# Kernel tuning notes

Hardware: AMD Instinct MI355X
Metric: run time of the kernel (lower is better)

## Reference

```python
import jax, jax.numpy as jnp
import numpy as np

B, T, FIN, D = 8, 512, 256, 128


def setup_inputs() -> dict:
    key = jax.random.key(0)
    ks = jax.random.split(key, 12)
    s = lambda fan_in: 1.0 / np.sqrt(fan_in)
    return {
        "x": jax.random.normal(ks[0], (B, T, FIN), jnp.float32),
        "S0": jnp.zeros((B, 1, D, D), jnp.float32),
        "Z0": jnp.zeros((B, 1, D), jnp.float32),
        "gamma": jnp.ones((FIN,), jnp.float32),
        "beta": jnp.zeros((FIN,), jnp.float32),
        "Wk": jax.random.normal(ks[1], (FIN, D), jnp.float32) * s(FIN),
        "Wq": jax.random.normal(ks[2], (FIN, D), jnp.float32) * s(FIN),
        "Wv": jax.random.normal(ks[3], (FIN, D), jnp.float32) * s(FIN),
        "W1": jax.random.normal(ks[4], (D, D), jnp.float32) * s(D),
        "b1": jnp.zeros((D,), jnp.float32),
        "W2": jax.random.normal(ks[5], (D, D), jnp.float32) * s(D),
        "b2": jnp.zeros((D,), jnp.float32),
        "Ws": jax.random.normal(ks[6], (FIN, D), jnp.float32) * s(FIN),
        "bs": jnp.zeros((D,), jnp.float32),
    }


def reference(x, S0, Z0, gamma, beta, Wk, Wq, Wv, W1, b1, W2, b2, Ws, bs):
    CLAMP = 1e20
    # LayerNorm over feature dim
    mu = jnp.mean(x, axis=-1, keepdims=True)
    var = jnp.var(x, axis=-1, keepdims=True)
    xn = (x - mu) / jnp.sqrt(var + 1e-5) * gamma + beta
    # phi(x) = elu(x) + 1
    K = jax.nn.elu(xn @ Wk) + 1.0  # [B,T,D]
    Q = jax.nn.elu(xn @ Wq) + 1.0  # [B,T,D]
    V = xn @ Wv                     # [B,T,D]
    # outer-product state recurrence via cumsum (faithful to original)
    outer = jnp.einsum('bti,btj->btij', K, V)            # [B,T,D,D]
    S = jnp.clip(jnp.cumsum(outer, axis=1), -CLAMP, CLAMP) + S0  # [B,T,D,D]
    Z = jnp.clip(jnp.cumsum(K, axis=1), -CLAMP, CLAMP) + Z0      # [B,T,D]
    numerator = jnp.einsum('bti,btil->btl', Q, S)        # [B,T,D]
    denominator = jnp.einsum('bti,bti->bt', Q, Z)[..., None] + 1e-5
    out = numerator / denominator
    # FFN: relu(relu(out W1 + b1) W2 + b2)
    out = jax.nn.relu(jax.nn.relu(out @ W1 + b1) @ W2 + b2)
    # residual shortcut from normed input
    out = out + xn @ Ws + bs
    S_out = S.reshape(B, T, D * D)
    return out, S_out, Z
```

## Files before the change

kernel.cpp:

```cpp
#include <hip/hip_runtime.h>


constexpr int BB = 8, TT = 512, FIN_ = 256, DD = 128;
constexpr int NROW = BB * TT;
constexpr int CLEN = 64, NCH = 8;
constexpr float CLAMPV = 1e20f;

typedef float f4v __attribute__((ext_vector_type(4)));

__global__ __launch_bounds__(256) void gemm_qkvs(
    const float* __restrict__ x,
    const float* __restrict__ gamma, const float* __restrict__ beta,
    const float* __restrict__ Wk, const float* __restrict__ Wq,
    const float* __restrict__ Wv, const float* __restrict__ Ws,
    const float* __restrict__ bs,
    float* __restrict__ Kb, float* __restrict__ Qb,
    float* __restrict__ Vb, float* __restrict__ Rb)
{
  int ct = blockIdx.x, rt = blockIdx.y;
  int mat = ct >> 1, cb = (ct & 1) * 64;
  const float* W = (mat == 0) ? Wk : (mat == 1) ? Wq : (mat == 2) ? Wv : Ws;
  float* Ob      = (mat == 0) ? Kb : (mat == 1) ? Qb : (mat == 2) ? Vb : Rb;
  __shared__ float As[2][16][64];
  __shared__ float Bs[2][16][64];
  __shared__ float mu_s[64], rs_s[64];
  int tid = threadIdx.x;
  {
    int row = tid >> 2, q = tid & 3;
    const float* xr = &x[(rt * 64 + row) * FIN_ + q * 64];
    float sum = 0.f, sq = 0.f;
#pragma unroll
    for (int u = 0; u < 16; u++) {
      float4 v = *(const float4*)&xr[u * 4];
      sum += v.x + v.y + v.z + v.w;
      sq  += v.x * v.x + v.y * v.y + v.z * v.z + v.w * v.w;
    }
    sum += __shfl_xor(sum, 1); sq += __shfl_xor(sq, 1);
    sum += __shfl_xor(sum, 2); sq += __shfl_xor(sq, 2);
    if (q == 0) {
      float mu = sum * (1.0f / FIN_);
      float var = sq * (1.0f / FIN_) - mu * mu;
      mu_s[row] = mu;
      rs_s[row] = rsqrtf(var + 1e-5f);
    }
  }
  __syncthreads();
  int tn = tid & 15, tm = tid >> 4;
  int lm = tid >> 2, lq = tid & 3;
  int lk = tid >> 4, ln4 = (tid & 15) * 4;
  float acc[4][4] = {};
  float mu = mu_s[lm], rs = rs_s[lm];
  float4 xa = *(const float4*)&x[(rt * 64 + lm) * FIN_ + lq * 4];
  float4 ga = *(const float4*)&gamma[lq * 4];
  float4 be = *(const float4*)&beta[lq * 4];
  float4 wb = *(const float4*)&W[lk * DD + cb + ln4];
  int cur = 0;
  for (int k0 = 0; k0 < FIN_; k0 += 16) {
    As[cur][lq * 4 + 0][lm] = (xa.x - mu) * rs * ga.x + be.x;
    As[cur][lq * 4 + 1][lm] = (xa.y - mu) * rs * ga.y + be.y;
    As[cur][lq * 4 + 2][lm] = (xa.z - mu) * rs * ga.z + be.z;
    As[cur][lq * 4 + 3][lm] = (xa.w - mu) * rs * ga.w + be.w;
    *(float4*)&Bs[cur][lk][ln4] = wb;
    if (k0 + 16 < FIN_) {
      xa = *(const float4*)&x[(rt * 64 + lm) * FIN_ + k0 + 16 + lq * 4];
      ga = *(const float4*)&gamma[k0 + 16 + lq * 4];
      be = *(const float4*)&beta[k0 + 16 + lq * 4];
      wb = *(const float4*)&W[(k0 + 16 + lk) * DD + cb + ln4];
    }
    __syncthreads();
#pragma unroll
    for (int k = 0; k < 16; k++) {
      float4 a = *(const float4*)&As[cur][k][tm * 4];
      float4 b = *(const float4*)&Bs[cur][k][tn * 4];
      float ar[4] = {a.x, a.y, a.z, a.w};
      float br[4] = {b.x, b.y, b.z, b.w};
#pragma unroll
      for (int i = 0; i < 4; i++)
#pragma unroll
        for (int j = 0; j < 4; j++) acc[i][j] += ar[i] * br[j];
    }
    cur ^= 1;
  }
#pragma unroll
  for (int i = 0; i < 4; i++) {
    int row = rt * 64 + tm * 4 + i;
    int col = cb + tn * 4;
    float vals[4];
#pragma unroll
    for (int j = 0; j < 4; j++) {
      float v = acc[i][j];
      if (mat <= 1) v = (v > 0.f) ? v + 1.f : expf(v);
      else if (mat == 3) v += bs[col + j];
      vals[j] = v;
    }
    *(float4*)&Ob[row * DD + col] = make_float4(vals[0], vals[1], vals[2], vals[3]);
  }
}

__global__ __launch_bounds__(256) void prefix_kernel(
    const float* __restrict__ Kb, const float* __restrict__ Vb,
    const float* __restrict__ S0, const float* __restrict__ Z0,
    float* __restrict__ prefS, float* __restrict__ prefz)
{
  int jt = blockIdx.x, it = blockIdx.y, b = blockIdx.z;
  int i0 = it * 16, j0 = jt * 32;
  __shared__ float Ks[2][CLEN][16];
  __shared__ float Vs[2][CLEN][32];
  int tid = threadIdx.x;
  int il = tid >> 4, jl = tid & 15;
  float2 s0v = *(const float2*)&S0[b * DD * DD + (i0 + il) * DD + j0 + jl * 2];
  float acc0 = 0.f, acc1 = 0.f;
  float zacc = 0.f;
  float z0v = (jt == 0 && tid < 16) ? Z0[b * DD + i0 + tid] : 0.f;
  {
    const float* Kc = Kb + (b * TT) * DD;
    const float* Vc = Vb + (b * TT) * DD;
    int t = tid >> 2, i4 = (tid & 3) * 4;
    *(float4*)&Ks[0][t][i4] = *(const float4*)&Kc[t * DD + i0 + i4];
#pragma unroll
    for (int u = 0; u < 2; u++) {
      int idx = u * 256 + tid;
      int tv = idx >> 3, j4 = (idx & 7) * 4;
      *(float4*)&Vs[0][tv][j4] = *(const float4*)&Vc[tv * DD + j0 + j4];
    }
  }
  int cur = 0;
  for (int c = 0; c < NCH; c++) {
    __syncthreads();
    float4 kq, vq0, vq1;
    if (c + 1 < NCH) {
      const float* Kc = Kb + (b * TT + (c + 1) * CLEN) * DD;
      const float* Vc = Vb + (b * TT + (c + 1) * CLEN) * DD;
      kq  = *(const float4*)&Kc[(tid >> 2) * DD + i0 + (tid & 3) * 4];
      vq0 = *(const float4*)&Vc[(tid >> 3) * DD + j0 + (tid & 7) * 4];
      int idx = 256 + tid;
      vq1 = *(const float4*)&Vc[(idx >> 3) * DD + j0 + (idx & 7) * 4];
    }
    float2 op = make_float2(acc0 + s0v.x, acc1 + s0v.y);
    *(float2*)&prefS[(size_t)(b * NCH + c) * DD * DD + (i0 + il) * DD + j0 + jl * 2] = op;
    if (jt == 0 && tid < 16)
      prefz[(b * NCH + c) * DD + i0 + tid] = zacc + z0v;
#pragma unroll 8
    for (int t = 0; t < CLEN; t++) {
      float k = Ks[cur][t][il];
      float2 v2 = *(const float2*)&Vs[cur][t][jl * 2];
      acc0 += k * v2.x;
      acc1 += k * v2.y;
    }
    if (jt == 0 && tid < 16) {
      float z = 0.f;
#pragma unroll 8
      for (int t = 0; t < CLEN; t++) z += Ks[cur][t][tid];
      zacc += z;
    }
    if (c + 1 < NCH) {
      *(float4*)&Ks[cur ^ 1][tid >> 2][(tid & 3) * 4] = kq;
      *(float4*)&Vs[cur ^ 1][tid >> 3][(tid & 7) * 4] = vq0;
      int idx = 256 + tid;
      *(float4*)&Vs[cur ^ 1][idx >> 3][(idx & 7) * 4] = vq1;
    }
    cur ^= 1;
  }
}

union MegaSmem {
  struct {
    float KsT[DD][CLEN + 2];
    float Qs[8][132];
    float sc[8][CLEN + 2];
    float zeff[DD];
    float den[8];
    float As[8][132];
    float H1[8][132];
  } a;
  struct {
    float Vs[CLEN][DD];
    float Ksm[CLEN][16];
  } s;
};

__global__ __launch_bounds__(256) void mega_kernel(
    const float* __restrict__ Kb, const float* __restrict__ Qb,
    const float* __restrict__ Vb, const float* __restrict__ prefS,
    const float* __restrict__ prefz, const float* __restrict__ Rb,
    const float* __restrict__ W1, const float* __restrict__ b1,
    const float* __restrict__ W2, const float* __restrict__ b2,
    float* __restrict__ Zout, float* __restrict__ out_main,
    float* __restrict__ Sout)
{
  __shared__ MegaSmem sm;
  int c = blockIdx.y, b = blockIdx.z, tid = threadIdx.x;
  const float* Kc = Kb + (b * TT + c * CLEN) * DD;
  const float* Vc = Vb + (b * TT + c * CLEN) * DD;

  if (blockIdx.x >= 8) {
    int i0 = (blockIdx.x - 8) * 16;
#pragma unroll
    for (int u = 0; u < 8; u++) {
      int idx = u * 256 + tid;
      int t = idx >> 5, c4 = (idx & 31) * 4;
      *(float4*)&sm.s.Vs[t][c4] = *(const float4*)&Vc[t * DD + c4];
    }
#pragma unroll
    for (int u = 0; u < 4; u++) {
      int idx = u * 256 + tid;
      int t = idx >> 4, r = idx & 15;
      sm.s.Ksm[t][r] = Kc[t * DD + i0 + r];
    }
    __syncthreads();
    int irow = tid >> 5, jq = tid & 31;
    int j = jq * 4;
    size_t pbase = (size_t)(b * NCH + c) * DD * DD;
    float4 prefA = *(const float4*)&prefS[pbase + (i0 + irow) * DD + j];
    float4 prefB = *(const float4*)&prefS[pbase + (i0 + 8 + irow) * DD + j];
    float4 accA = make_float4(0.f, 0.f, 0.f, 0.f);
    float4 accB = make_float4(0.f, 0.f, 0.f, 0.f);
    float* SoA = Sout + (size_t)(b * TT + c * CLEN) * (DD * DD) + (i0 + irow) * DD + j;
    float* SoB = SoA + 8 * DD;
#pragma unroll 2
    for (int t = 0; t < CLEN; t++) {
      float4 v4 = *(const float4*)&sm.s.Vs[t][j];
      float kA = sm.s.Ksm[t][irow];
      float kB = sm.s.Ksm[t][irow + 8];
      accA.x += kA * v4.x; accA.y += kA * v4.y;
      accA.z += kA * v4.z; accA.w += kA * v4.w;
      f4v oA;
      oA.x = fminf(fmaxf(prefA.x + accA.x, -CLAMPV), CLAMPV);
      oA.y = fminf(fmaxf(prefA.y + accA.y, -CLAMPV), CLAMPV);
      oA.z = fminf(fmaxf(prefA.z + accA.z, -CLAMPV), CLAMPV);
      oA.w = fminf(fmaxf(prefA.w + accA.w, -CLAMPV), CLAMPV);
      __builtin_nontemporal_store(oA, (f4v*)&SoA[(size_t)t * (DD * DD)]);
      accB.x += kB * v4.x; accB.y += kB * v4.y;
      accB.z += kB * v4.z; accB.w += kB * v4.w;
      f4v oB;
      oB.x = fminf(fmaxf(prefB.x + accB.x, -CLAMPV), CLAMPV);
      oB.y = fminf(fmaxf(prefB.y + accB.y, -CLAMPV), CLAMPV);
      oB.z = fminf(fmaxf(prefB.z + accB.z, -CLAMPV), CLAMPV);
      oB.w = fminf(fmaxf(prefB.w + accB.w, -CLAMPV), CLAMPV);
      __builtin_nontemporal_store(oB, (f4v*)&SoB[(size_t)t * (DD * DD)]);
    }
    return;
  }

  int sub = blockIdx.x;
  int t0 = sub * 8;
  int tlim = t0 + 8;
  const float* Qc = Qb + (b * TT + c * CLEN) * DD;
  for (int idx = tid; idx < tlim * 32; idx += 256) {
    int t = idx >> 5, c4 = (idx & 31) * 4;
    float4 vv = *(const float4*)&Kc[t * DD + c4];
    sm.a.KsT[c4 + 0][t] = vv.x; sm.a.KsT[c4 + 1][t] = vv.y;
    sm.a.KsT[c4 + 2][t] = vv.z; sm.a.KsT[c4 + 3][t] = vv.w;
  }
  {
    int r = tid >> 5, c4 = (tid & 31) * 4;
    *(float4*)&sm.a.Qs[r][c4] = *(const float4*)&Qc[(t0 + r) * DD + c4];
  }
  if (tid < DD) sm.a.zeff[tid] = prefz[(b * NCH + c) * DD + tid];
  __syncthreads();
  {
    int tm = tid >> 5, tn = tid & 31;
    int tau0 = tn * 2;
    if (tau0 < tlim) {
      float s0 = 0.f, s1 = 0.f;
#pragma unroll 8
      for (int k = 0; k < DD; k++) {
        float q = sm.a.Qs[tm][k];
        float2 kk = *(const float2*)&sm.a.KsT[k][tau0];
        s0 += q * kk.x;
        s1 += q * kk.y;
      }
      int t = t0 + tm;
      sm.a.sc[tm][tau0]     = (tau0     <= t) ? s0 : 0.f;
      sm.a.sc[tm][tau0 + 1] = (tau0 + 1 <= t) ? s1 : 0.f;
    }
  }
  __syncthreads();
  {
    int r = tid >> 5, g = tid & 31;
    int t = t0 + r;
    float p = 0.f;
    for (int tau = g; tau <= t; tau += 32) p += sm.a.sc[r][tau];
#pragma unroll 4
    for (int k = g; k < DD; k += 32) p += sm.a.Qs[r][k] * sm.a.zeff[k];
#pragma unroll
    for (int off = 1; off < 32; off <<= 1) p += __shfl_xor(p, off);
    if (g == 0) sm.a.den[r] = p + 1e-5f;
  }
  __syncthreads();
  int tl = tid & 31, r = tid >> 5;
  int l0 = tl * 4;
  {
    float n0[4] = {};
#pragma unroll 4
    for (int tau = 0; tau < tlim; tau++) {
      float4 v4 = *(const float4*)&Vc[tau * DD + l0];
      float s = sm.a.sc[r][tau];
      n0[0] += s * v4.x; n0[1] += s * v4.y; n0[2] += s * v4.z; n0[3] += s * v4.w;
    }
    const float* P = prefS + (size_t)(b * NCH + c) * DD * DD;
#pragma unroll 4
    for (int i = 0; i < DD; i++) {
      float4 p4 = *(const float4*)&P[i * DD + l0];
      float q = sm.a.Qs[r][i];
      n0[0] += q * p4.x; n0[1] += q * p4.y; n0[2] += q * p4.z; n0[3] += q * p4.w;
    }
    float dd = sm.a.den[r];
    *(float4*)&sm.a.As[r][l0] =
        make_float4(n0[0] / dd, n0[1] / dd, n0[2] / dd, n0[3] / dd);
  }
  if (sub == 7 && tid < DD) {
    int i = tid;
    float a = sm.a.zeff[i];
    for (int t = 0; t < CLEN; t++) {
      a += sm.a.KsT[i][t];
      a = fminf(fmaxf(a, -CLAMPV), CLAMPV);
      __builtin_nontemporal_store(a, &Zout[(size_t)(b * TT + c * CLEN + t) * DD + i]);
    }
  }
  __syncthreads();
  {
    float a1[4] = {};
#pragma unroll 8
    for (int k = 0; k < DD; k++) {
      float4 w = *(const float4*)&W1[k * DD + l0];
      float a = sm.a.As[r][k];
      a1[0] += a * w.x; a1[1] += a * w.y; a1[2] += a * w.z; a1[3] += a * w.w;
    }
    float4 bv = *(const float4*)&b1[l0];
    float4 h;
    h.x = fmaxf(a1[0] + bv.x, 0.f);
    h.y = fmaxf(a1[1] + bv.y, 0.f);
    h.z = fmaxf(a1[2] + bv.z, 0.f);
    h.w = fmaxf(a1[3] + bv.w, 0.f);
    *(float4*)&sm.a.H1[r][l0] = h;
  }
  __syncthreads();
  {
    float a2[4] = {};
#pragma unroll 8
    for (int k = 0; k < DD; k++) {
      float4 w = *(const float4*)&W2[k * DD + l0];
      float a = sm.a.H1[r][k];
      a2[0] += a * w.x; a2[1] += a * w.y; a2[2] += a * w.z; a2[3] += a * w.w;
    }
    int grow = b * TT + c * CLEN + t0 + r;
    float4 b2v = *(const float4*)&b2[l0];
    float4 rv = *(const float4*)&Rb[grow * DD + l0];
    float4 o;
    o.x = fmaxf(a2[0] + b2v.x, 0.f) + rv.x;
    o.y = fmaxf(a2[1] + b2v.y, 0.f) + rv.y;
    o.z = fmaxf(a2[2] + b2v.z, 0.f) + rv.z;
    o.w = fmaxf(a2[3] + b2v.w, 0.f) + rv.w;
    *(float4*)&out_main[grow * DD + l0] = o;
  }
}

extern "C" void kernel_launch(void* const* d_in, const int* in_sizes, int n_in,
                              void* d_out, int out_size, void* d_ws, size_t ws_size,
                              hipStream_t stream)
{
  const float* x     = (const float*)d_in[0];
  const float* S0    = (const float*)d_in[1];
  const float* Z0    = (const float*)d_in[2];
  const float* gamma = (const float*)d_in[3];
  const float* beta  = (const float*)d_in[4];
  const float* Wk    = (const float*)d_in[5];
  const float* Wq    = (const float*)d_in[6];
  const float* Wv    = (const float*)d_in[7];
  const float* W1    = (const float*)d_in[8];
  const float* b1    = (const float*)d_in[9];
  const float* W2    = (const float*)d_in[10];
  const float* b2    = (const float*)d_in[11];
  const float* Ws    = (const float*)d_in[12];
  const float* bs    = (const float*)d_in[13];

  float* out_main = (float*)d_out;
  float* Sout = out_main + NROW * DD;
  float* Zout = Sout + (size_t)NROW * DD * DD;

  float* ws_f   = (float*)d_ws;
  float* Kb     = ws_f;
  float* Qb     = Kb + 524288;
  float* Vb     = Qb + 524288;
  float* Rb     = Vb + 524288;
  float* prefS  = Rb + 524288;
  float* prefz  = prefS + 1048576;

  gemm_qkvs<<<dim3(8, 64), 256, 0, stream>>>(x, gamma, beta, Wk, Wq, Wv, Ws, bs,
                                             Kb, Qb, Vb, Rb);
  prefix_kernel<<<dim3(4, 8, BB), 256, 0, stream>>>(Kb, Vb, S0, Z0, prefS, prefz);
  mega_kernel<<<dim3(16, NCH, BB), 256, 0, stream>>>(Kb, Qb, Vb, prefS, prefz, Rb,
                                                     W1, b1, W2, b2,
                                                     Zout, out_main, Sout);
}
```

Baseline: 373.9 us.

## Fuse S-state output writes into prefix scan kernel, drop S blocks from mega kernel

Moves the per-timestep cumulative state writes into the chunk-sequential prefix kernel, which now also emits the clamped running sum for every timestep. The mega kernel loses its state-writing blocks and becomes an attention/FFN-only kernel. The prefix grid is retiled to 8x64 tiles with 256 blocks. The aim is to avoid reloading the chunk prefix, at the cost of serialising the large output write across chunks within each block and using narrower float2 stores.

```diff
diff --git a/kernel.cpp b/kernel.cpp
--- a/kernel.cpp
+++ b/kernel.cpp
@@ -7,6 +7,7 @@
 constexpr float CLAMPV = 1e20f;
 
 typedef float f4v __attribute__((ext_vector_type(4)));
+typedef float f2v __attribute__((ext_vector_type(2)));
 
 __global__ __launch_bounds__(256) void gemm_qkvs(
     const float* __restrict__ x,
@@ -100,148 +101,99 @@
 __global__ __launch_bounds__(256) void prefix_kernel(
     const float* __restrict__ Kb, const float* __restrict__ Vb,
     const float* __restrict__ S0, const float* __restrict__ Z0,
-    float* __restrict__ prefS, float* __restrict__ prefz)
+    float* __restrict__ prefS, float* __restrict__ prefz,
+    float* __restrict__ Sout)
 {
-  int jt = blockIdx.x, it = blockIdx.y, b = blockIdx.z;
-  int i0 = it * 16, j0 = jt * 32;
-  __shared__ float Ks[2][CLEN][16];
-  __shared__ float Vs[2][CLEN][32];
+  int jh = blockIdx.x, it = blockIdx.y, b = blockIdx.z;
+  int i0 = it * 8, j0 = jh * 64;
+  __shared__ float Ks[2][CLEN][8];
+  __shared__ float Vs[2][CLEN][64];
   int tid = threadIdx.x;
-  int il = tid >> 4, jl = tid & 15;
+  int il = tid >> 5, jl = tid & 31;
   float2 s0v = *(const float2*)&S0[b * DD * DD + (i0 + il) * DD + j0 + jl * 2];
-  float acc0 = 0.f, acc1 = 0.f;
-  float zacc = 0.f;
-  float z0v = (jt == 0 && tid < 16) ? Z0[b * DD + i0 + tid] : 0.f;
+  float acc0 = 0.f, acc1 = 0.f, zacc = 0.f;
+  float z0v = (jh == 0 && tid < 8) ? Z0[b * DD + i0 + tid] : 0.f;
   {
     const float* Kc = Kb + (b * TT) * DD;
     const float* Vc = Vb + (b * TT) * DD;
-    int t = tid >> 2, i4 = (tid & 3) * 4;
-    *(float4*)&Ks[0][t][i4] = *(const float4*)&Kc[t * DD + i0 + i4];
-#pragma unroll
-    for (int u = 0; u < 2; u++) {
+    int t = tid >> 2, i2 = (tid & 3) * 2;
+    *(float2*)&Ks[0][t][i2] = *(const float2*)&Kc[t * DD + i0 + i2];
+#pragma unroll
+    for (int u = 0; u < 4; u++) {
       int idx = u * 256 + tid;
-      int tv = idx >> 3, j4 = (idx & 7) * 4;
+      int tv = idx >> 4, j4 = (idx & 15) * 4;
       *(float4*)&Vs[0][tv][j4] = *(const float4*)&Vc[tv * DD + j0 + j4];
     }
   }
   int cur = 0;
   for (int c = 0; c < NCH; c++) {
     __syncthreads();
-    float4 kq, vq0, vq1;
+    float2 kq;
+    float4 vq[4];
     if (c + 1 < NCH) {
       const float* Kc = Kb + (b * TT + (c + 1) * CLEN) * DD;
       const float* Vc = Vb + (b * TT + (c + 1) * CLEN) * DD;
-      kq  = *(const float4*)&Kc[(tid >> 2) * DD + i0 + (tid & 3) * 4];
-      vq0 = *(const float4*)&Vc[(tid >> 3) * DD + j0 + (tid & 7) * 4];
-      int idx = 256 + tid;
-      vq1 = *(const float4*)&Vc[(idx >> 3) * DD + j0 + (idx & 7) * 4];
-    }
-    float2 op = make_float2(acc0 + s0v.x, acc1 + s0v.y);
-    *(float2*)&prefS[(size_t)(b * NCH + c) * DD * DD + (i0 + il) * DD + j0 + jl * 2] = op;
-    if (jt == 0 && tid < 16)
+      kq = *(const float2*)&Kc[(tid >> 2) * DD + i0 + (tid & 3) * 2];
+#pragma unroll
+      for (int u = 0; u < 4; u++) {
+        int idx = u * 256 + tid;
+        vq[u] = *(const float4*)&Vc[(idx >> 4) * DD + j0 + (idx & 15) * 4];
+      }
+    }
+    float p0 = acc0 + s0v.x, p1 = acc1 + s0v.y;
+    *(float2*)&prefS[(size_t)(b * NCH + c) * DD * DD + (i0 + il) * DD + j0 + jl * 2] =
+        make_float2(p0, p1);
+    if (jh == 0 && tid < 8)
       prefz[(b * NCH + c) * DD + i0 + tid] = zacc + z0v;
-#pragma unroll 8
+    float w0 = 0.f, w1 = 0.f;
+    float* So = Sout + (size_t)(b * TT + c * CLEN) * (DD * DD) + (i0 + il) * DD + j0 + jl * 2;
+#pragma unroll 4
     for (int t = 0; t < CLEN; t++) {
       float k = Ks[cur][t][il];
       float2 v2 = *(const float2*)&Vs[cur][t][jl * 2];
-      acc0 += k * v2.x;
-      acc1 += k * v2.y;
-    }
-    if (jt == 0 && tid < 16) {
+      acc0 += k * v2.x; acc1 += k * v2.y;
+      w0 += k * v2.x;   w1 += k * v2.y;
+      f2v o2;
+      o2.x = fminf(fmaxf(p0 + w0, -CLAMPV), CLAMPV);
+      o2.y = fminf(fmaxf(p1 + w1, -CLAMPV), CLAMPV);
+      __builtin_nontemporal_store(o2, (f2v*)&So[(size_t)t * (DD * DD)]);
+    }
+    if (jh == 0 && tid < 8) {
       float z = 0.f;
 #pragma unroll 8
       for (int t = 0; t < CLEN; t++) z += Ks[cur][t][tid];
       zacc += z;
     }
     if (c + 1 < NCH) {
-      *(float4*)&Ks[cur ^ 1][tid >> 2][(tid & 3) * 4] = kq;
-      *(float4*)&Vs[cur ^ 1][tid >> 3][(tid & 7) * 4] = vq0;
-      int idx = 256 + tid;
-      *(float4*)&Vs[cur ^ 1][idx >> 3][(idx & 7) * 4] = vq1;
+      *(float2*)&Ks[cur ^ 1][tid >> 2][(tid & 3) * 2] = kq;
+#pragma unroll
+      for (int u = 0; u < 4; u++) {
+        int idx = u * 256 + tid;
+        *(float4*)&Vs[cur ^ 1][idx >> 4][(idx & 15) * 4] = vq[u];
+      }
     }
     cur ^= 1;
   }
 }
 
-union MegaSmem {
-  struct {
-    float KsT[DD][CLEN + 2];
-    float Qs[8][132];
-    float sc[8][CLEN + 2];
-    float zeff[DD];
-    float den[8];
-    float As[8][132];
-    float H1[8][132];
-  } a;
-  struct {
-    float Vs[CLEN][DD];
-    float Ksm[CLEN][16];
-  } s;
-};
-
-__global__ __launch_bounds__(256) void mega_kernel(
+__global__ __launch_bounds__(256) void attn_kernel(
     const float* __restrict__ Kb, const float* __restrict__ Qb,
     const float* __restrict__ Vb, const float* __restrict__ prefS,
     const float* __restrict__ prefz, const float* __restrict__ Rb,
     const float* __restrict__ W1, const float* __restrict__ b1,
     const float* __restrict__ W2, const float* __restrict__ b2,
-    float* __restrict__ Zout, float* __restrict__ out_main,
-    float* __restrict__ Sout)
+    float* __restrict__ Zout, float* __restrict__ out_main)
 {
-  __shared__ MegaSmem sm;
+  __shared__ float KsT[DD][CLEN + 2];
+  __shared__ float Qs[8][132];
+  __shared__ float sc[8][CLEN + 2];
+  __shared__ float zeff[DD];
+  __shared__ float den[8];
+  __shared__ float Ao[8][132];
+  __shared__ float H1[8][132];
   int c = blockIdx.y, b = blockIdx.z, tid = threadIdx.x;
   const float* Kc = Kb + (b * TT + c * CLEN) * DD;
   const float* Vc = Vb + (b * TT + c * CLEN) * DD;
-
-  if (blockIdx.x >= 8) {
-    int i0 = (blockIdx.x - 8) * 16;
-#pragma unroll
-    for (int u = 0; u < 8; u++) {
-      int idx = u * 256 + tid;
-      int t = idx >> 5, c4 = (idx & 31) * 4;
-      *(float4*)&sm.s.Vs[t][c4] = *(const float4*)&Vc[t * DD + c4];
-    }
-#pragma unroll
-    for (int u = 0; u < 4; u++) {
-      int idx = u * 256 + tid;
-      int t = idx >> 4, r = idx & 15;
-      sm.s.Ksm[t][r] = Kc[t * DD + i0 + r];
-    }
-    __syncthreads();
-    int irow = tid >> 5, jq = tid & 31;
-    int j = jq * 4;
-    size_t pbase = (size_t)(b * NCH + c) * DD * DD;
-    float4 prefA = *(const float4*)&prefS[pbase + (i0 + irow) * DD + j];
-    float4 prefB = *(const float4*)&prefS[pbase + (i0 + 8 + irow) * DD + j];
-    float4 accA = make_float4(0.f, 0.f, 0.f, 0.f);
-    float4 accB = make_float4(0.f, 0.f, 0.f, 0.f);
-    float* SoA = Sout + (size_t)(b * TT + c * CLEN) * (DD * DD) + (i0 + irow) * DD + j;
-    float* SoB = SoA + 8 * DD;
-#pragma unroll 2
-    for (int t = 0; t < CLEN; t++) {
-      float4 v4 = *(const float4*)&sm.s.Vs[t][j];
-      float kA = sm.s.Ksm[t][irow];
-      float kB = sm.s.Ksm[t][irow + 8];
-      accA.x += kA * v4.x; accA.y += kA * v4.y;
-      accA.z += kA * v4.z; accA.w += kA * v4.w;
-      f4v oA;
-      oA.x = fminf(fmaxf(prefA.x + accA.x, -CLAMPV), CLAMPV);
-      oA.y = fminf(fmaxf(prefA.y + accA.y, -CLAMPV), CLAMPV);
-      oA.z = fminf(fmaxf(prefA.z + accA.z, -CLAMPV), CLAMPV);
-      oA.w = fminf(fmaxf(prefA.w + accA.w, -CLAMPV), CLAMPV);
-      __builtin_nontemporal_store(oA, (f4v*)&SoA[(size_t)t * (DD * DD)]);
-      accB.x += kB * v4.x; accB.y += kB * v4.y;
-      accB.z += kB * v4.z; accB.w += kB * v4.w;
-      f4v oB;
-      oB.x = fminf(fmaxf(prefB.x + accB.x, -CLAMPV), CLAMPV);
-      oB.y = fminf(fmaxf(prefB.y + accB.y, -CLAMPV), CLAMPV);
-      oB.z = fminf(fmaxf(prefB.z + accB.z, -CLAMPV), CLAMPV);
-      oB.w = fminf(fmaxf(prefB.w + accB.w, -CLAMPV), CLAMPV);
-      __builtin_nontemporal_store(oB, (f4v*)&SoB[(size_t)t * (DD * DD)]);
-    }
-    return;
-  }
-
   int sub = blockIdx.x;
   int t0 = sub * 8;
   int tlim = t0 + 8;
@@ -249,14 +201,14 @@
   for (int idx = tid; idx < tlim * 32; idx += 256) {
     int t = idx >> 5, c4 = (idx & 31) * 4;
     float4 vv = *(const float4*)&Kc[t * DD + c4];
-    sm.a.KsT[c4 + 0][t] = vv.x; sm.a.KsT[c4 + 1][t] = vv.y;
-    sm.a.KsT[c4 + 2][t] = vv.z; sm.a.KsT[c4 + 3][t] = vv.w;
+    KsT[c4 + 0][t] = vv.x; KsT[c4 + 1][t] = vv.y;
+    KsT[c4 + 2][t] = vv.z; KsT[c4 + 3][t] = vv.w;
   }
   {
     int r = tid >> 5, c4 = (tid & 31) * 4;
-    *(float4*)&sm.a.Qs[r][c4] = *(const float4*)&Qc[(t0 + r) * DD + c4];
-  }
-  if (tid < DD) sm.a.zeff[tid] = prefz[(b * NCH + c) * DD + tid];
+    *(float4*)&Qs[r][c4] = *(const float4*)&Qc[(t0 + r) * DD + c4];
+  }
+  if (tid < DD) zeff[tid] = prefz[(b * NCH + c) * DD + tid];
   __syncthreads();
   {
     int tm = tid >> 5, tn = tid & 31;
@@ -265,14 +217,14 @@
       float s0 = 0.f, s1 = 0.f;
 #pragma unroll 8
       for (int k = 0; k < DD; k++) {
-        float q = sm.a.Qs[tm][k];
-        float2 kk = *(const float2*)&sm.a.KsT[k][tau0];
+        float q = Qs[tm][k];
+        float2 kk = *(const float2*)&KsT[k][tau0];
         s0 += q * kk.x;
         s1 += q * kk.y;
       }
       int t = t0 + tm;
-      sm.a.sc[tm][tau0]     = (tau0     <= t) ? s0 : 0.f;
-      sm.a.sc[tm][tau0 + 1] = (tau0 + 1 <= t) ? s1 : 0.f;
+      sc[tm][tau0]     = (tau0     <= t) ? s0 : 0.f;
+      sc[tm][tau0 + 1] = (tau0 + 1 <= t) ? s1 : 0.f;
     }
   }
   __syncthreads();
@@ -280,12 +232,12 @@
     int r = tid >> 5, g = tid & 31;
     int t = t0 + r;
     float p = 0.f;
-    for (int tau = g; tau <= t; tau += 32) p += sm.a.sc[r][tau];
+    for (int tau = g; tau <= t; tau += 32) p += sc[r][tau];
 #pragma unroll 4
-    for (int k = g; k < DD; k += 32) p += sm.a.Qs[r][k] * sm.a.zeff[k];
+    for (int k = g; k < DD; k += 32) p += Qs[r][k] * zeff[k];
 #pragma unroll
     for (int off = 1; off < 32; off <<= 1) p += __shfl_xor(p, off);
-    if (g == 0) sm.a.den[r] = p + 1e-5f;
+    if (g == 0) den[r] = p + 1e-5f;
   }
   __syncthreads();
   int tl = tid & 31, r = tid >> 5;
@@ -295,25 +247,24 @@
 #pragma unroll 4
     for (int tau = 0; tau < tlim; tau++) {
       float4 v4 = *(const float4*)&Vc[tau * DD + l0];
-      float s = sm.a.sc[r][tau];
+      float s = sc[r][tau];
       n0[0] += s * v4.x; n0[1] += s * v4.y; n0[2] += s * v4.z; n0[3] += s * v4.w;
     }
     const float* P = prefS + (size_t)(b * NCH + c) * DD * DD;
 #pragma unroll 4
     for (int i = 0; i < DD; i++) {
       float4 p4 = *(const float4*)&P[i * DD + l0];
-      float q = sm.a.Qs[r][i];
+      float q = Qs[r][i];
       n0[0] += q * p4.x; n0[1] += q * p4.y; n0[2] += q * p4.z; n0[3] += q * p4.w;
     }
-    float dd = sm.a.den[r];
-    *(float4*)&sm.a.As[r][l0] =
-        make_float4(n0[0] / dd, n0[1] / dd, n0[2] / dd, n0[3] / dd);
+    float dd = den[r];
+    *(float4*)&Ao[r][l0] = make_float4(n0[0] / dd, n0[1] / dd, n0[2] / dd, n0[3] / dd);
   }
   if (sub == 7 && tid < DD) {
     int i = tid;
-    float a = sm.a.zeff[i];
+    float a = zeff[i];
     for (int t = 0; t < CLEN; t++) {
-      a += sm.a.KsT[i][t];
+      a += KsT[i][t];
       a = fminf(fmaxf(a, -CLAMPV), CLAMPV);
       __builtin_nontemporal_store(a, &Zout[(size_t)(b * TT + c * CLEN + t) * DD + i]);
     }
@@ -324,7 +275,7 @@
 #pragma unroll 8
     for (int k = 0; k < DD; k++) {
       float4 w = *(const float4*)&W1[k * DD + l0];
-      float a = sm.a.As[r][k];
+      float a = Ao[r][k];
       a1[0] += a * w.x; a1[1] += a * w.y; a1[2] += a * w.z; a1[3] += a * w.w;
     }
     float4 bv = *(const float4*)&b1[l0];
@@ -333,7 +284,7 @@
     h.y = fmaxf(a1[1] + bv.y, 0.f);
     h.z = fmaxf(a1[2] + bv.z, 0.f);
     h.w = fmaxf(a1[3] + bv.w, 0.f);
-    *(float4*)&sm.a.H1[r][l0] = h;
+    *(float4*)&H1[r][l0] = h;
   }
   __syncthreads();
   {
@@ -341,7 +292,7 @@
 #pragma unroll 8
     for (int k = 0; k < DD; k++) {
       float4 w = *(const float4*)&W2[k * DD + l0];
-      float a = sm.a.H1[r][k];
+      float a = H1[r][k];
       a2[0] += a * w.x; a2[1] += a * w.y; a2[2] += a * w.z; a2[3] += a * w.w;
     }
     int grow = b * TT + c * CLEN + t0 + r;
@@ -389,8 +340,7 @@
 
   gemm_qkvs<<<dim3(8, 64), 256, 0, stream>>>(x, gamma, beta, Wk, Wq, Wv, Ws, bs,
                                              Kb, Qb, Vb, Rb);
-  prefix_kernel<<<dim3(4, 8, BB), 256, 0, stream>>>(Kb, Vb, S0, Z0, prefS, prefz);
-  mega_kernel<<<dim3(16, NCH, BB), 256, 0, stream>>>(Kb, Qb, Vb, prefS, prefz, Rb,
-                                                     W1, b1, W2, b2,
-                                                     Zout, out_main, Sout);
+  prefix_kernel<<<dim3(2, 16, BB), 256, 0, stream>>>(Kb, Vb, S0, Z0, prefS, prefz, Sout);
+  attn_kernel<<<dim3(8, NCH, BB), 256, 0, stream>>>(Kb, Qb, Vb, prefS, prefz, Rb,
+                                                    W1, b1, W2, b2, Zout, out_main);
 }
```

Result: faster. 364.2 us, median of 2 (-2.6%).

## Write first half of S output inside prefix kernel, skip in mega kernel

Applied to the files above, without the earlier changes.

The prefix kernel now also writes the full per-timestep clamped S state for the first WSPLIT chunks while it scans, and the mega kernel's S-writing blocks exit early for those chunks. The prefix kernel tiling changes from 16x32 to 8x64 (i by j) per block, giving 256 blocks. The aim is to spread the large S output write (about 268MB) across two kernels so the bandwidth-bound store starts earlier and the mega kernel has less to write. The cost is that the prefix kernel, which was short, now carries heavy store traffic for its chunks serially over c, so its blocks run longer.

```diff
diff --git a/kernel.cpp b/kernel.cpp
--- a/kernel.cpp
+++ b/kernel.cpp
@@ -4,9 +4,11 @@
 constexpr int BB = 8, TT = 512, FIN_ = 256, DD = 128;
 constexpr int NROW = BB * TT;
 constexpr int CLEN = 64, NCH = 8;
+constexpr int WSPLIT = 4;
 constexpr float CLAMPV = 1e20f;
 
 typedef float f4v __attribute__((ext_vector_type(4)));
+typedef float f2v __attribute__((ext_vector_type(2)));
 
 __global__ __launch_bounds__(256) void gemm_qkvs(
     const float* __restrict__ x,
@@ -100,64 +102,85 @@
 __global__ __launch_bounds__(256) void prefix_kernel(
     const float* __restrict__ Kb, const float* __restrict__ Vb,
     const float* __restrict__ S0, const float* __restrict__ Z0,
-    float* __restrict__ prefS, float* __restrict__ prefz)
+    float* __restrict__ prefS, float* __restrict__ prefz,
+    float* __restrict__ Sout)
 {
-  int jt = blockIdx.x, it = blockIdx.y, b = blockIdx.z;
-  int i0 = it * 16, j0 = jt * 32;
-  __shared__ float Ks[2][CLEN][16];
-  __shared__ float Vs[2][CLEN][32];
+  int jh = blockIdx.x, it = blockIdx.y, b = blockIdx.z;
+  int i0 = it * 8, j0 = jh * 64;
+  __shared__ float Ks[2][CLEN][8];
+  __shared__ float Vs[2][CLEN][64];
   int tid = threadIdx.x;
-  int il = tid >> 4, jl = tid & 15;
+  int il = tid >> 5, jl = tid & 31;
   float2 s0v = *(const float2*)&S0[b * DD * DD + (i0 + il) * DD + j0 + jl * 2];
-  float acc0 = 0.f, acc1 = 0.f;
-  float zacc = 0.f;
-  float z0v = (jt == 0 && tid < 16) ? Z0[b * DD + i0 + tid] : 0.f;
+  float acc0 = 0.f, acc1 = 0.f, zacc = 0.f;
+  float z0v = (jh == 0 && tid < 8) ? Z0[b * DD + i0 + tid] : 0.f;
   {
     const float* Kc = Kb + (b * TT) * DD;
     const float* Vc = Vb + (b * TT) * DD;
-    int t = tid >> 2, i4 = (tid & 3) * 4;
-    *(float4*)&Ks[0][t][i4] = *(const float4*)&Kc[t * DD + i0 + i4];
-#pragma unroll
-    for (int u = 0; u < 2; u++) {
+    int t = tid >> 2, i2 = (tid & 3) * 2;
+    *(float2*)&Ks[0][t][i2] = *(const float2*)&Kc[t * DD + i0 + i2];
+#pragma unroll
+    for (int u = 0; u < 4; u++) {
       int idx = u * 256 + tid;
-      int tv = idx >> 3, j4 = (idx & 7) * 4;
+      int tv = idx >> 4, j4 = (idx & 15) * 4;
       *(float4*)&Vs[0][tv][j4] = *(const float4*)&Vc[tv * DD + j0 + j4];
     }
   }
   int cur = 0;
   for (int c = 0; c < NCH; c++) {
     __syncthreads();
-    float4 kq, vq0, vq1;
+    float2 kq;
+    float4 vq[4];
     if (c + 1 < NCH) {
       const float* Kc = Kb + (b * TT + (c + 1) * CLEN) * DD;
       const float* Vc = Vb + (b * TT + (c + 1) * CLEN) * DD;
-      kq  = *(const float4*)&Kc[(tid >> 2) * DD + i0 + (tid & 3) * 4];
-      vq0 = *(const float4*)&Vc[(tid >> 3) * DD + j0 + (tid & 7) * 4];
-      int idx = 256 + tid;
-      vq1 = *(const float4*)&Vc[(idx >> 3) * DD + j0 + (idx & 7) * 4];
-    }
-    float2 op = make_float2(acc0 + s0v.x, acc1 + s0v.y);
-    *(float2*)&prefS[(size_t)(b * NCH + c) * DD * DD + (i0 + il) * DD + j0 + jl * 2] = op;
-    if (jt == 0 && tid < 16)
+      kq = *(const float2*)&Kc[(tid >> 2) * DD + i0 + (tid & 3) * 2];
+#pragma unroll
+      for (int u = 0; u < 4; u++) {
+        int idx = u * 256 + tid;
+        vq[u] = *(const float4*)&Vc[(idx >> 4) * DD + j0 + (idx & 15) * 4];
+      }
+    }
+    float p0 = acc0 + s0v.x, p1 = acc1 + s0v.y;
+    *(float2*)&prefS[(size_t)(b * NCH + c) * DD * DD + (i0 + il) * DD + j0 + jl * 2] =
+        make_float2(p0, p1);
+    if (jh == 0 && tid < 8)
       prefz[(b * NCH + c) * DD + i0 + tid] = zacc + z0v;
+    if (c < WSPLIT) {
+      float w0 = 0.f, w1 = 0.f;
+      float* So = Sout + (size_t)(b * TT + c * CLEN) * (DD * DD) + (i0 + il) * DD + j0 + jl * 2;
+#pragma unroll 4
+      for (int t = 0; t < CLEN; t++) {
+        float k = Ks[cur][t][il];
+        float2 v2 = *(const float2*)&Vs[cur][t][jl * 2];
+        acc0 += k * v2.x; acc1 += k * v2.y;
+        w0 += k * v2.x;   w1 += k * v2.y;
+        f2v o2;
+        o2.x = fminf(fmaxf(p0 + w0, -CLAMPV), CLAMPV);
+        o2.y = fminf(fmaxf(p1 + w1, -CLAMPV), CLAMPV);
+        __builtin_nontemporal_store(o2, (f2v*)&So[(size_t)t * (DD * DD)]);
+      }
+    } else {
 #pragma unroll 8
-    for (int t = 0; t < CLEN; t++) {
-      float k = Ks[cur][t][il];
-      float2 v2 = *(const float2*)&Vs[cur][t][jl * 2];
-      acc0 += k * v2.x;
-      acc1 += k * v2.y;
-    }
-    if (jt == 0 && tid < 16) {
+      for (int t = 0; t < CLEN; t++) {
+        float k = Ks[cur][t][il];
+        float2 v2 = *(const float2*)&Vs[cur][t][jl * 2];
+        acc0 += k * v2.x; acc1 += k * v2.y;
+      }
+    }
+    if (jh == 0 && tid < 8) {
       float z = 0.f;
 #pragma unroll 8
       for (int t = 0; t < CLEN; t++) z += Ks[cur][t][tid];
       zacc += z;
     }
     if (c + 1 < NCH) {
-      *(float4*)&Ks[cur ^ 1][tid >> 2][(tid & 3) * 4] = kq;
-      *(float4*)&Vs[cur ^ 1][tid >> 3][(tid & 7) * 4] = vq0;
-      int idx = 256 + tid;
-      *(float4*)&Vs[cur ^ 1][idx >> 3][(idx & 7) * 4] = vq1;
+      *(float2*)&Ks[cur ^ 1][tid >> 2][(tid & 3) * 2] = kq;
+#pragma unroll
+      for (int u = 0; u < 4; u++) {
+        int idx = u * 256 + tid;
+        *(float4*)&Vs[cur ^ 1][idx >> 4][(idx & 15) * 4] = vq[u];
+      }
     }
     cur ^= 1;
   }
@@ -170,7 +193,7 @@
     float sc[8][CLEN + 2];
     float zeff[DD];
     float den[8];
-    float As[8][132];
+    float Ao[8][132];
     float H1[8][132];
   } a;
   struct {
@@ -194,6 +217,7 @@
   const float* Vc = Vb + (b * TT + c * CLEN) * DD;
 
   if (blockIdx.x >= 8) {
+    if (c < WSPLIT) return;
     int i0 = (blockIdx.x - 8) * 16;
 #pragma unroll
     for (int u = 0; u < 8; u++) {
@@ -306,8 +330,7 @@
       n0[0] += q * p4.x; n0[1] += q * p4.y; n0[2] += q * p4.z; n0[3] += q * p4.w;
     }
     float dd = sm.a.den[r];
-    *(float4*)&sm.a.As[r][l0] =
-        make_float4(n0[0] / dd, n0[1] / dd, n0[2] / dd, n0[3] / dd);
+    *(float4*)&sm.a.Ao[r][l0] = make_float4(n0[0] / dd, n0[1] / dd, n0[2] / dd, n0[3] / dd);
   }
   if (sub == 7 && tid < DD) {
     int i = tid;
@@ -324,7 +347,7 @@
 #pragma unroll 8
     for (int k = 0; k < DD; k++) {
       float4 w = *(const float4*)&W1[k * DD + l0];
-      float a = sm.a.As[r][k];
+      float a = sm.a.Ao[r][k];
       a1[0] += a * w.x; a1[1] += a * w.y; a1[2] += a * w.z; a1[3] += a * w.w;
     }
     float4 bv = *(const float4*)&b1[l0];
@@ -389,7 +412,7 @@
 
   gemm_qkvs<<<dim3(8, 64), 256, 0, stream>>>(x, gamma, beta, Wk, Wq, Wv, Ws, bs,
                                              Kb, Qb, Vb, Rb);
-  prefix_kernel<<<dim3(4, 8, BB), 256, 0, stream>>>(Kb, Vb, S0, Z0, prefS, prefz);
+  prefix_kernel<<<dim3(2, 16, BB), 256, 0, stream>>>(Kb, Vb, S0, Z0, prefS, prefz, Sout);
   mega_kernel<<<dim3(16, NCH, BB), 256, 0, stream>>>(Kb, Qb, Vb, prefS, prefz, Rb,
                                                      W1, b1, W2, b2,
                                                      Zout, out_main, Sout);
```

Result: slower. 392.4 us (+4.9%).
